# Kernel tuning notes

Hardware: AMD Instinct MI355X
Metric: run time of the kernel (lower is better)

Reference implementation:

```python
import jax, jax.numpy as jnp
import numpy as np

W, H, C = 4096, 4096, 3


def setup_inputs() -> dict:
    key = jax.random.key(0)
    k_img, k_perm = jax.random.split(key)
    image = jax.random.normal(k_img, (W, H, C), dtype=jnp.float32)
    # Per-pixel random permutation of channels: argsort of iid uniforms along C
    # reproduces np.random.permutation(c) at every (i, j) deterministically.
    noise = jax.random.uniform(k_perm, (W, H, C))
    perm = jnp.argsort(noise, axis=-1).astype(jnp.int32)  # [W, H, C]
    return {"image": image, "perm": perm}


def reference(image, perm):
    # out[i, j, k] = image[i, j, perm[i, j, k]]  (per-pixel channel gather)
    return jnp.take_along_axis(image, perm, axis=-1)
```

## Files before the change

### kernel.cpp

```cpp
#include <hip/hip_runtime.h>


__global__ __launch_bounds__(256) void PerPixelChannelPermutation_kernel(
    const float4* __restrict__ img4, const int4* __restrict__ perm4,
    float4* __restrict__ out4, int nthreads) {
    int t = blockIdx.x * blockDim.x + threadIdx.x;
    if (t >= nthreads) return;
    int base = t * 3;

    float4 i0 = img4[base + 0];
    float4 i1 = img4[base + 1];
    float4 i2 = img4[base + 2];
    int4   q0 = perm4[base + 0];
    int4   q1 = perm4[base + 1];
    int4   q2 = perm4[base + 2];

    float a[12] = {i0.x, i0.y, i0.z, i0.w,
                   i1.x, i1.y, i1.z, i1.w,
                   i2.x, i2.y, i2.z, i2.w};
    int   p[12] = {q0.x, q0.y, q0.z, q0.w,
                   q1.x, q1.y, q1.z, q1.w,
                   q2.x, q2.y, q2.z, q2.w};
    float o[12];

#pragma unroll
    for (int px = 0; px < 4; ++px) {
        const float c0 = a[3 * px + 0];
        const float c1 = a[3 * px + 1];
        const float c2 = a[3 * px + 2];
#pragma unroll
        for (int k = 0; k < 3; ++k) {
            const int pk = p[3 * px + k];
            o[3 * px + k] = (pk == 0) ? c0 : ((pk == 1) ? c1 : c2);
        }
    }

    out4[base + 0] = make_float4(o[0], o[1], o[2], o[3]);
    out4[base + 1] = make_float4(o[4], o[5], o[6], o[7]);
    out4[base + 2] = make_float4(o[8], o[9], o[10], o[11]);
}

extern "C" void kernel_launch(void* const* d_in, const int* in_sizes, int n_in,
                              void* d_out, int out_size, void* d_ws, size_t ws_size,
                              hipStream_t stream) {
    const float4* img4  = (const float4*)d_in[0];
    const int4*   perm4 = (const int4*)d_in[1];
    float4*       out4  = (float4*)d_out;

    const int n_elems  = in_sizes[0];
    const int nthreads = n_elems / 12;

    const int block = 256;
    const int grid  = (nthreads + block - 1) / block;
    PerPixelChannelPermutation_kernel<<<grid, block, 0, stream>>>(
        img4, perm4, out4, nthreads);
}
```

Before: 436.4 us.

## Process two chunks per thread and use nontemporal stores for output

Each thread now handles two 12-float chunks, one from each half of the array, so more loads are in flight per thread and the grid is halved. Output writes use nontemporal stores to avoid polluting the cache with write-once data. The kernel assumes the chunk count is even; an odd count would leave the last chunk unprocessed.

Measured after the change: 467.8 us. 1.07x slower.

```diff
diff --git a/kernel.cpp b/kernel.cpp
--- a/kernel.cpp
+++ b/kernel.cpp
@@ -1,57 +1,83 @@
 #include <hip/hip_runtime.h>
 
 
+typedef float f32x4 __attribute__((ext_vector_type(4)));
+typedef int   i32x4 __attribute__((ext_vector_type(4)));
+
+__device__ __forceinline__ float sel3(float a, float b, float c, int p) {
+    return (p == 0) ? a : ((p == 1) ? b : c);
+}
+
 __global__ __launch_bounds__(256) void PerPixelChannelPermutation_kernel(
-    const float4* __restrict__ img4, const int4* __restrict__ perm4,
-    float4* __restrict__ out4, int nthreads) {
-    int t = blockIdx.x * blockDim.x + threadIdx.x;
-    if (t >= nthreads) return;
-    int base = t * 3;
+    const f32x4* __restrict__ img4, const i32x4* __restrict__ perm4,
+    f32x4* __restrict__ out4, int half_chunks) {
+    const int t = blockIdx.x * blockDim.x + threadIdx.x;
+    if (t >= half_chunks) return;
+    const long baseA = (long)t * 3;
+    const long baseB = (long)(t + half_chunks) * 3;
 
-    float4 i0 = img4[base + 0];
-    float4 i1 = img4[base + 1];
-    float4 i2 = img4[base + 2];
-    int4   q0 = perm4[base + 0];
-    int4   q1 = perm4[base + 1];
-    int4   q2 = perm4[base + 2];
+    const f32x4 a0 = img4[baseA + 0];
+    const f32x4 a1 = img4[baseA + 1];
+    const f32x4 a2 = img4[baseA + 2];
+    const f32x4 b0 = img4[baseB + 0];
+    const f32x4 b1 = img4[baseB + 1];
+    const f32x4 b2 = img4[baseB + 2];
+    const i32x4 pa0 = perm4[baseA + 0];
+    const i32x4 pa1 = perm4[baseA + 1];
+    const i32x4 pa2 = perm4[baseA + 2];
+    const i32x4 pb0 = perm4[baseB + 0];
+    const i32x4 pb1 = perm4[baseB + 1];
+    const i32x4 pb2 = perm4[baseB + 2];
 
-    float a[12] = {i0.x, i0.y, i0.z, i0.w,
-                   i1.x, i1.y, i1.z, i1.w,
-                   i2.x, i2.y, i2.z, i2.w};
-    int   p[12] = {q0.x, q0.y, q0.z, q0.w,
-                   q1.x, q1.y, q1.z, q1.w,
-                   q2.x, q2.y, q2.z, q2.w};
-    float o[12];
+    f32x4 oa0, oa1, oa2, ob0, ob1, ob2;
 
-#pragma unroll
-    for (int px = 0; px < 4; ++px) {
-        const float c0 = a[3 * px + 0];
-        const float c1 = a[3 * px + 1];
-        const float c2 = a[3 * px + 2];
-#pragma unroll
-        for (int k = 0; k < 3; ++k) {
-            const int pk = p[3 * px + k];
-            o[3 * px + k] = (pk == 0) ? c0 : ((pk == 1) ? c1 : c2);
-        }
-    }
+    oa0.x = sel3(a0.x, a0.y, a0.z, pa0.x);
+    oa0.y = sel3(a0.x, a0.y, a0.z, pa0.y);
+    oa0.z = sel3(a0.x, a0.y, a0.z, pa0.z);
+    oa0.w = sel3(a0.w, a1.x, a1.y, pa0.w);
+    oa1.x = sel3(a0.w, a1.x, a1.y, pa1.x);
+    oa1.y = sel3(a0.w, a1.x, a1.y, pa1.y);
+    oa1.z = sel3(a1.z, a1.w, a2.x, pa1.z);
+    oa1.w = sel3(a1.z, a1.w, a2.x, pa1.w);
+    oa2.x = sel3(a1.z, a1.w, a2.x, pa2.x);
+    oa2.y = sel3(a2.y, a2.z, a2.w, pa2.y);
+    oa2.z = sel3(a2.y, a2.z, a2.w, pa2.z);
+    oa2.w = sel3(a2.y, a2.z, a2.w, pa2.w);
 
-    out4[base + 0] = make_float4(o[0], o[1], o[2], o[3]);
-    out4[base + 1] = make_float4(o[4], o[5], o[6], o[7]);
-    out4[base + 2] = make_float4(o[8], o[9], o[10], o[11]);
+    ob0.x = sel3(b0.x, b0.y, b0.z, pb0.x);
+    ob0.y = sel3(b0.x, b0.y, b0.z, pb0.y);
+    ob0.z = sel3(b0.x, b0.y, b0.z, pb0.z);
+    ob0.w = sel3(b0.w, b1.x, b1.y, pb0.w);
+    ob1.x = sel3(b0.w, b1.x, b1.y, pb1.x);
+    ob1.y = sel3(b0.w, b1.x, b1.y, pb1.y);
+    ob1.z = sel3(b1.z, b1.w, b2.x, pb1.z);
+    ob1.w = sel3(b1.z, b1.w, b2.x, pb1.w);
+    ob2.x = sel3(b1.z, b1.w, b2.x, pb2.x);
+    ob2.y = sel3(b2.y, b2.z, b2.w, pb2.y);
+    ob2.z = sel3(b2.y, b2.z, b2.w, pb2.z);
+    ob2.w = sel3(b2.y, b2.z, b2.w, pb2.w);
+
+    __builtin_nontemporal_store(oa0, &out4[baseA + 0]);
+    __builtin_nontemporal_store(oa1, &out4[baseA + 1]);
+    __builtin_nontemporal_store(oa2, &out4[baseA + 2]);
+    __builtin_nontemporal_store(ob0, &out4[baseB + 0]);
+    __builtin_nontemporal_store(ob1, &out4[baseB + 1]);
+    __builtin_nontemporal_store(ob2, &out4[baseB + 2]);
 }
 
 extern "C" void kernel_launch(void* const* d_in, const int* in_sizes, int n_in,
                               void* d_out, int out_size, void* d_ws, size_t ws_size,
                               hipStream_t stream) {
-    const float4* img4  = (const float4*)d_in[0];
-    const int4*   perm4 = (const int4*)d_in[1];
-    float4*       out4  = (float4*)d_out;
+    const f32x4* img4  = (const f32x4*)d_in[0];
+    const i32x4* perm4 = (const i32x4*)d_in[1];
+    f32x4*       out4  = (f32x4*)d_out;
 
-    const int n_elems  = in_sizes[0];
-    const int nthreads = n_elems / 12;
+    const int n_elems     = in_sizes[0];
+    const int n_chunks    = n_elems / 12;
+    const int half_chunks = n_chunks / 2;
 
     const int block = 256;
-    const int grid  = (nthreads + block - 1) / block;
+    const int grid  = (half_chunks + block - 1) / block;
     PerPixelChannelPermutation_kernel<<<grid, block, 0, stream>>>(
-        img4, perm4, out4, nthreads);
+        img4, perm4, out4, half_chunks);
 }
```

## Process one float4 per thread using lane shuffles to fetch neighboring pixel channels

Applied to the files above, without the earlier changes.

Each thread now handles a single 4-float chunk instead of four whole pixels (three float4s). Pixel channels that straddle chunk boundaries are fetched from neighbouring lanes with shuffle up/down, and lanes at the wavefront edges fall back to scalar global loads. Each output comes from an 8-way select indexed by the pixel's start offset plus the permutation value. The aim is fully coalesced contiguous float4 accesses across a wavefront, in place of the stride-48-byte per-thread pattern, at the cost of extra shuffles, integer divides and edge-lane branches.

Measured after the change: 427.6 us. -2.0%, faster.

```diff
diff --git a/kernel.cpp b/kernel.cpp
--- a/kernel.cpp
+++ b/kernel.cpp
@@ -1,57 +1,86 @@
 #include <hip/hip_runtime.h>
 
 
+typedef float f32x4 __attribute__((ext_vector_type(4)));
+typedef int   i32x4 __attribute__((ext_vector_type(4)));
+
+__device__ __forceinline__ float sel8(float c0, float c1, float c2, float c3,
+                                      float c4, float c5, float c6, float c7,
+                                      int idx) {
+    float s01 = (idx & 1) ? c1 : c0;
+    float s23 = (idx & 1) ? c3 : c2;
+    float s45 = (idx & 1) ? c5 : c4;
+    float s67 = (idx & 1) ? c7 : c6;
+    float s03 = (idx & 2) ? s23 : s01;
+    float s47 = (idx & 2) ? s67 : s45;
+    return (idx & 4) ? s47 : s03;
+}
+
 __global__ __launch_bounds__(256) void PerPixelChannelPermutation_kernel(
-    const float4* __restrict__ img4, const int4* __restrict__ perm4,
-    float4* __restrict__ out4, int nthreads) {
-    int t = blockIdx.x * blockDim.x + threadIdx.x;
-    if (t >= nthreads) return;
-    int base = t * 3;
+    const float* __restrict__ img, const i32x4* __restrict__ perm4,
+    f32x4* __restrict__ out4, int nchunks, int n_elems) {
+    const int c = blockIdx.x * blockDim.x + threadIdx.x;
+    if (c >= nchunks) return;
+    const int c4 = c * 4;
 
-    float4 i0 = img4[base + 0];
-    float4 i1 = img4[base + 1];
-    float4 i2 = img4[base + 2];
-    int4   q0 = perm4[base + 0];
-    int4   q1 = perm4[base + 1];
-    int4   q2 = perm4[base + 2];
+    const f32x4* img4 = (const f32x4*)img;
+    const f32x4 v = img4[c];
+    const i32x4 q = perm4[c];
 
-    float a[12] = {i0.x, i0.y, i0.z, i0.w,
-                   i1.x, i1.y, i1.z, i1.w,
-                   i2.x, i2.y, i2.z, i2.w};
-    int   p[12] = {q0.x, q0.y, q0.z, q0.w,
-                   q1.x, q1.y, q1.z, q1.w,
-                   q2.x, q2.y, q2.z, q2.w};
-    float o[12];
+    float pm2 = __shfl_up(v.z, 1);
+    float pm1 = __shfl_up(v.w, 1);
+    float nx0 = __shfl_down(v.x, 1);
+    float nx1 = __shfl_down(v.y, 1);
 
-#pragma unroll
-    for (int px = 0; px < 4; ++px) {
-        const float c0 = a[3 * px + 0];
-        const float c1 = a[3 * px + 1];
-        const float c2 = a[3 * px + 2];
-#pragma unroll
-        for (int k = 0; k < 3; ++k) {
-            const int pk = p[3 * px + k];
-            o[3 * px + k] = (pk == 0) ? c0 : ((pk == 1) ? c1 : c2);
-        }
+    const int lane = threadIdx.x & 63;
+    if (lane == 0) {
+        int b = c4 - 2; if (b < 0) b = 0;
+        pm2 = img[b];
+        pm1 = img[b + 1];
+    }
+    if (lane == 63) {
+        int b = c4 + 4; if (b > n_elems - 2) b = n_elems - 2;
+        nx0 = img[b];
+        nx1 = img[b + 1];
     }
 
-    out4[base + 0] = make_float4(o[0], o[1], o[2], o[3]);
-    out4[base + 1] = make_float4(o[4], o[5], o[6], o[7]);
-    out4[base + 2] = make_float4(o[8], o[9], o[10], o[11]);
+    f32x4 o;
+    {
+        const unsigned n = (unsigned)(c4 + 0);
+        const int idx = (int)((n / 3u) * 3u) - c4 + 2 + q.x;
+        o.x = sel8(pm2, pm1, v.x, v.y, v.z, v.w, nx0, nx1, idx);
+    }
+    {
+        const unsigned n = (unsigned)(c4 + 1);
+        const int idx = (int)((n / 3u) * 3u) - c4 + 2 + q.y;
+        o.y = sel8(pm2, pm1, v.x, v.y, v.z, v.w, nx0, nx1, idx);
+    }
+    {
+        const unsigned n = (unsigned)(c4 + 2);
+        const int idx = (int)((n / 3u) * 3u) - c4 + 2 + q.z;
+        o.z = sel8(pm2, pm1, v.x, v.y, v.z, v.w, nx0, nx1, idx);
+    }
+    {
+        const unsigned n = (unsigned)(c4 + 3);
+        const int idx = (int)((n / 3u) * 3u) - c4 + 2 + q.w;
+        o.w = sel8(pm2, pm1, v.x, v.y, v.z, v.w, nx0, nx1, idx);
+    }
+
+    out4[c] = o;
 }
 
 extern "C" void kernel_launch(void* const* d_in, const int* in_sizes, int n_in,
                               void* d_out, int out_size, void* d_ws, size_t ws_size,
                               hipStream_t stream) {
-    const float4* img4  = (const float4*)d_in[0];
-    const int4*   perm4 = (const int4*)d_in[1];
-    float4*       out4  = (float4*)d_out;
+    const float* img   = (const float*)d_in[0];
+    const i32x4* perm4 = (const i32x4*)d_in[1];
+    f32x4*       out4  = (f32x4*)d_out;
 
-    const int n_elems  = in_sizes[0];
-    const int nthreads = n_elems / 12;
+    const int n_elems = in_sizes[0];
+    const int nchunks = n_elems / 4;
 
     const int block = 256;
-    const int grid  = (nthreads + block - 1) / block;
+    const int grid  = (nchunks + block - 1) / block;
     PerPixelChannelPermutation_kernel<<<grid, block, 0, stream>>>(
-        img4, perm4, out4, nthreads);
+        img, perm4, out4, nchunks, n_elems);
 }
```
